# Kernel tuning notes

Hardware: AMD Instinct MI355X
Metric: run time of the kernel (lower is better)

The kernel has to match this reference:

```python
import jax, jax.numpy as jnp
import numpy as np

N_NODES = 100000
N_EDGES = 3200000
IN_DIM = 3
HID = 8
OUT_DIM = 1


def setup_inputs() -> dict:
    key = jax.random.key(0)
    ks = jax.random.split(key, 10)
    x = jax.random.normal(ks[0], (N_NODES, IN_DIM), dtype=jnp.float32)
    edge_index = jax.random.randint(ks[1], (2, N_EDGES), 0, N_NODES, dtype=jnp.int64)
    cat_dim = 2 * (HID + IN_DIM)  # 22
    s = lambda fan_in: 1.0 / np.sqrt(fan_in)
    W_in = jax.random.uniform(ks[2], (IN_DIM, HID), jnp.float32, -s(IN_DIM), s(IN_DIM))
    b_in = jnp.zeros((HID,), jnp.float32)
    W1 = jax.random.uniform(ks[3], (cat_dim, HID), jnp.float32, -s(cat_dim), s(cat_dim))
    b1 = jnp.zeros((HID,), jnp.float32)
    W2 = jax.random.uniform(ks[4], (HID, HID), jnp.float32, -s(HID), s(HID))
    b2 = jnp.zeros((HID,), jnp.float32)
    W_e = jax.random.uniform(ks[5], (cat_dim, OUT_DIM), jnp.float32, -s(cat_dim), s(cat_dim))
    b_e = jnp.zeros((OUT_DIM,), jnp.float32)
    return {"x": x, "edge_index": edge_index, "W_in": W_in, "b_in": b_in,
            "W1": W1, "b1": b1, "W2": W2, "b2": b2, "W_e": W_e, "b_e": b_e}


def reference(x, edge_index, W_in, b_in, W1, b1, W2, b2, W_e, b_e):
    src = edge_index[0]  # j (source)
    dst = edge_index[1]  # i (target)

    # inputnet: Linear + Tanh
    H = jnp.tanh(x @ W_in + b_in)               # [N, HID]
    feat = jnp.concatenate([H, x], axis=-1)      # [N, HID+IN_DIM]

    # One EdgeConv iteration (n_iters=1): message = nn(cat([x_i, x_j - x_i]))
    xi = feat[dst]                                # [E, 11]
    xj = feat[src]                                # [E, 11]
    e = jnp.concatenate([xi, xj - xi], axis=-1)   # [E, 22]
    m = jax.nn.sigmoid(e @ W1 + b1)               # [E, HID]
    m = jax.nn.sigmoid(m @ W2 + b2)               # [E, HID]
    H = jax.ops.segment_sum(m, dst, num_segments=N_NODES)  # scatter-add to targets
    feat = jnp.concatenate([H, x], axis=-1)       # [N, 11]

    # edgenetwork on concatenated endpoint features
    ef = jnp.concatenate([feat[src], feat[dst]], axis=-1)   # [E, 22]
    out = jax.nn.sigmoid(ef @ W_e + b_e)          # [E, 1]
    return out.squeeze(-1)                        # [E]
```

## Files before the change

kernel.cpp:

```cpp
#include <hip/hip_runtime.h>
#include <hip/hip_fp16.h>

#define TPB     256
#define BSH     9
#define BW      512
#define EPB     8192
#define NBMAX   256
#define S_SPLIT 16
#define FXS     2097152.0f
#define FXSI    (1.0f / 2097152.0f)

static __device__ __forceinline__ float sigmoidf(float v) {
    return __builtin_amdgcn_rcpf(1.0f + __expf(-v));
}

static __device__ __forceinline__ void unpack8(uint4 u, float o[8]) {
    union { unsigned int u; __half2 h; } c0, c1, c2, c3;
    c0.u = u.x; c1.u = u.y; c2.u = u.z; c3.u = u.w;
    float2 f0 = __half22float2(c0.h), f1 = __half22float2(c1.h);
    float2 f2 = __half22float2(c2.h), f3 = __half22float2(c3.h);
    o[0]=f0.x; o[1]=f0.y; o[2]=f1.x; o[3]=f1.y;
    o[4]=f2.x; o[5]=f2.y; o[6]=f3.x; o[7]=f3.y;
}

__global__ void k_prep(const float* __restrict__ x,
                       const float* __restrict__ W_in,
                       const float* __restrict__ b_in,
                       const float* __restrict__ W1,
                       const float* __restrict__ b1,
                       float* __restrict__ gi,
                       __half* __restrict__ gjh,
                       const int* __restrict__ dst,
                       int* __restrict__ raw,
                       int n_nodes, int n_edges, int NB, int NBLK) {
    __shared__ int cnt[NBMAX];
    int t = threadIdx.x;
    if ((int)blockIdx.x < NBLK) {
        for (int b = t; b < NB; b += TPB) cnt[b] = 0;
        __syncthreads();
        int e0 = blockIdx.x * EPB;
#pragma unroll
        for (int k = 0; k < EPB / (TPB * 4); ++k) {
            int e = e0 + k * TPB * 4 + t * 4;
            if (e + 3 < n_edges) {
                int4 d4 = *(const int4*)(dst + e);
                atomicAdd(&cnt[d4.x >> BSH], 1);
                atomicAdd(&cnt[d4.y >> BSH], 1);
                atomicAdd(&cnt[d4.z >> BSH], 1);
                atomicAdd(&cnt[d4.w >> BSH], 1);
            } else {
                int qe = min(e + 4, n_edges);
                for (int q = e; q < qe; ++q)
                    atomicAdd(&cnt[dst[q] >> BSH], 1);
            }
        }
        __syncthreads();
        for (int b = t; b < NB; b += TPB)
            raw[(size_t)blockIdx.x * NB + b] = cnt[b];
    } else {
        int n = ((int)blockIdx.x - NBLK) * TPB + t;
        if (n >= n_nodes) return;
        float x0 = x[3*n], x1 = x[3*n+1], x2 = x[3*n+2];
        float f[11];
#pragma unroll
        for (int c = 0; c < 8; ++c)
            f[c] = tanhf(b_in[c] + x0*W_in[c] + x1*W_in[8+c] + x2*W_in[16+c]);
        f[8] = x0; f[9] = x1; f[10] = x2;
        float giv[8], gjv[8];
#pragma unroll
        for (int h = 0; h < 8; ++h) {
            float vi = b1[h], vj = 0.0f;
#pragma unroll
            for (int k = 0; k < 11; ++k) {
                float wa = W1[k*8+h], wb = W1[(11+k)*8+h];
                vi += f[k] * (wa - wb);
                vj += f[k] * wb;
            }
            giv[h] = vi; gjv[h] = vj;
        }
        float4* gip = (float4*)(gi + (size_t)n * 8);
        gip[0] = make_float4(giv[0], giv[1], giv[2], giv[3]);
        gip[1] = make_float4(giv[4], giv[5], giv[6], giv[7]);
        __align__(16) __half hj[8];
#pragma unroll
        for (int k = 0; k < 8; ++k) hj[k] = __float2half_rn(gjv[k]);
        *(uint4*)(gjh + (size_t)n * 8) = *(const uint4*)hj;
    }
}

__global__ void k_scan_cols(const int* __restrict__ raw, int* __restrict__ rel,
                            int* __restrict__ totals, int NB, int NBLK) {
    __shared__ int s[TPB];
    int b = blockIdx.x, t = threadIdx.x;
    int carry = 0;
    for (int q = 0; q < NBLK; q += TPB) {
        int blk = q + t;
        int v = (blk < NBLK) ? raw[(size_t)blk * NB + b] : 0;
        __syncthreads();
        s[t] = v; __syncthreads();
        for (int o = 1; o < TPB; o <<= 1) {
            int u = (t >= o) ? s[t - o] : 0;
            __syncthreads();
            s[t] += u;
            __syncthreads();
        }
        if (blk < NBLK) rel[(size_t)blk * NB + b] = carry + s[t] - v;
        carry += s[TPB - 1];
    }
    if (t == 0) totals[b] = carry;
}

static __device__ __forceinline__ void base_scan(const int* __restrict__ totals,
                                                 int* s, int* sbase, int NB, int t) {
    int v = (t < NB) ? ((totals[t] + 3) & ~3) : 0;
    s[t] = v; __syncthreads();
    for (int o = 1; o < TPB; o <<= 1) {
        int u = (t >= o) ? s[t - o] : 0;
        __syncthreads();
        s[t] += u;
        __syncthreads();
    }
    if (t < NB) sbase[t] = s[t] - v;
    __syncthreads();
}

__launch_bounds__(TPB)
__global__ void k_scatter(const int* __restrict__ src, const int* __restrict__ dst,
                          const int* __restrict__ raw, const int* __restrict__ rel,
                          const int* __restrict__ totals,
                          int* __restrict__ sorted, int n_edges, int NB) {
    __shared__ int stage[EPB];
    __shared__ int cnt[NBMAX];
    __shared__ int lscan[NBMAX];
    __shared__ int gd[NBMAX];
    __shared__ int sbase[NBMAX];
    __shared__ int s[TPB];
    int t = threadIdx.x;

    base_scan(totals, s, sbase, NB, t);

    {
        int v = (t < NB) ? raw[(size_t)blockIdx.x * NB + t] : 0;
        __syncthreads();
        s[t] = v; __syncthreads();
        for (int o = 1; o < TPB; o <<= 1) {
            int u = (t >= o) ? s[t - o] : 0;
            __syncthreads();
            s[t] += u;
            __syncthreads();
        }
        if (t < NB) {
            lscan[t] = s[t] - v;
            cnt[t]   = s[t] - v;
            gd[t]    = sbase[t] + rel[(size_t)blockIdx.x * NB + t];
        }
    }
    __syncthreads();

    int e0 = blockIdx.x * EPB;
#pragma unroll
    for (int k = 0; k < EPB / (TPB * 4); ++k) {
        int e = e0 + k * TPB * 4 + t * 4;
        if (e + 3 < n_edges) {
            int4 s4 = *(const int4*)(src + e);
            int4 d4 = *(const int4*)(dst + e);
            int p;
            p = atomicAdd(&cnt[d4.x >> BSH], 1); stage[p] = (s4.x << BSH) | (d4.x & (BW-1));
            p = atomicAdd(&cnt[d4.y >> BSH], 1); stage[p] = (s4.y << BSH) | (d4.y & (BW-1));
            p = atomicAdd(&cnt[d4.z >> BSH], 1); stage[p] = (s4.z << BSH) | (d4.z & (BW-1));
            p = atomicAdd(&cnt[d4.w >> BSH], 1); stage[p] = (s4.w << BSH) | (d4.w & (BW-1));
        } else {
            int qe = min(e + 4, n_edges);
            for (int q = e; q < qe; ++q) {
                int d = dst[q];
                int p = atomicAdd(&cnt[d >> BSH], 1);
                stage[p] = (src[q] << BSH) | (d & (BW - 1));
            }
        }
    }
    __syncthreads();

    int wid = t >> 6, lane = t & 63;
    for (int b = wid; b < NB; b += (TPB / 64)) {
        int ls = lscan[b];
        int le = cnt[b];
        int g0 = gd[b];
        for (int i = ls + lane; i < le; i += 64)
            sorted[g0 + (i - ls)] = stage[i];
    }
}

__launch_bounds__(TPB, 4)
__global__ void k_bucket(const int* __restrict__ sorted,
                         const int* __restrict__ totals,
                         const float* __restrict__ gi, const __half* __restrict__ gjh,
                         const float* __restrict__ W2, const float* __restrict__ b2,
                         const float* __restrict__ W_e,
                         float* __restrict__ part, int n_nodes, int NB, int NBP) {
    __shared__ int sa[BW], sc[BW];
    __shared__ int sbase[NBMAX];
    __shared__ int s[TPB];
    int t = threadIdx.x;
    int sl = blockIdx.x / NBP;
    int b  = blockIdx.x - sl * NBP;

    base_scan(totals, s, sbase, NB, t);
    if (b >= NB) return;

    int nb0 = b * BW;
    for (int i = t; i < BW; i += TPB) { sa[i] = 0; sc[i] = 0; }
    __syncthreads();

    int beg = sbase[b];
    int len = totals[b];
    int qs = (((len + S_SPLIT - 1) / S_SPLIT) + 3) & ~3;
    int s0 = beg + sl * qs;
    int s1 = min(beg + len, s0 + qs);

    for (int g = s0 + t * 4; g < s1; g += TPB * 4) {
        if (g + 4 <= s1) {
            int4 pp = *(const int4*)(sorted + g);
            int d[4]  = { pp.x & (BW-1), pp.y & (BW-1), pp.z & (BW-1), pp.w & (BW-1) };
            int sj[4] = { pp.x >> BSH,   pp.y >> BSH,   pp.z >> BSH,   pp.w >> BSH };
            float ej[4][8];
#pragma unroll
            for (int q = 0; q < 4; ++q)
                unpack8(*(const uint4*)(gjh + (size_t)sj[q] * 8), ej[q]);
            float m[4][8];
#pragma unroll
            for (int q = 0; q < 4; ++q) {
                const float4* ip = (const float4*)(gi + (size_t)(nb0 + d[q]) * 8);
                float4 A = ip[0], B = ip[1];
                float ei[8] = {A.x,A.y,A.z,A.w,B.x,B.y,B.z,B.w};
#pragma unroll
                for (int k = 0; k < 8; ++k)
                    m[q][k] = sigmoidf(ei[k] + ej[q][k]);
            }
            float pa[4] = {0,0,0,0}, pc[4] = {0,0,0,0};
#pragma unroll
            for (int h = 0; h < 8; ++h) {
                float bb = b2[h];
                float v[4] = {bb, bb, bb, bb};
#pragma unroll
                for (int k = 0; k < 8; ++k) {
                    float w = W2[k*8+h];
#pragma unroll
                    for (int q = 0; q < 4; ++q) v[q] += m[q][k] * w;
                }
                float wa = W_e[h], wc = W_e[11+h];
#pragma unroll
                for (int q = 0; q < 4; ++q) {
                    float z = sigmoidf(v[q]);
                    pa[q] += z * wa; pc[q] += z * wc;
                }
            }
#pragma unroll
            for (int q = 0; q < 4; ++q) {
                atomicAdd(&sa[d[q]], __float2int_rn(pa[q] * FXS));
                atomicAdd(&sc[d[q]], __float2int_rn(pc[q] * FXS));
            }
        } else {
            for (int e = g; e < s1; ++e) {
                int p = sorted[e];
                int dl = p & (BW - 1);
                float ej[8];
                unpack8(*(const uint4*)(gjh + (size_t)(p >> BSH) * 8), ej);
                const float4* ip = (const float4*)(gi + (size_t)(nb0 + dl) * 8);
                float4 A = ip[0], B = ip[1];
                float ei[8] = {A.x,A.y,A.z,A.w,B.x,B.y,B.z,B.w};
                float m[8];
#pragma unroll
                for (int k = 0; k < 8; ++k) m[k] = sigmoidf(ei[k] + ej[k]);
                float pa = 0, pc = 0;
#pragma unroll
                for (int h = 0; h < 8; ++h) {
                    float v = b2[h];
#pragma unroll
                    for (int k = 0; k < 8; ++k) v += m[k] * W2[k*8+h];
                    float z = sigmoidf(v);
                    pa += z * W_e[h]; pc += z * W_e[11+h];
                }
                atomicAdd(&sa[dl], __float2int_rn(pa * FXS));
                atomicAdd(&sc[dl], __float2int_rn(pc * FXS));
            }
        }
    }
    __syncthreads();
    size_t row = (size_t)blockIdx.x * (2 * BW);
    for (int i = t; i < BW; i += TPB) {
        part[row + i]      = (float)sa[i] * FXSI;
        part[row + BW + i] = (float)sc[i] * FXSI;
    }
}

__global__ void k_acc(const float* __restrict__ part, const float* __restrict__ x,
                      const float* __restrict__ W_e, float* __restrict__ ac,
                      int n_nodes, int NBP) {
    int n = blockIdx.x * blockDim.x + threadIdx.x;
    if (n >= n_nodes) return;
    int b = n >> BSH, r = n & (BW - 1);
    float a = 0.0f, c = 0.0f;
#pragma unroll
    for (int s = 0; s < S_SPLIT; ++s) {
        const float* pp = part + ((size_t)(s * NBP + b)) * (2 * BW);
        a += pp[r];
        c += pp[BW + r];
    }
    float x0 = x[3*n], x1 = x[3*n+1], x2 = x[3*n+2];
    a += x0 * W_e[8]  + x1 * W_e[9]  + x2 * W_e[10];
    c += x0 * W_e[19] + x1 * W_e[20] + x2 * W_e[21];
    ac[2*n]     = a;
    ac[2*n + 1] = c;
}

__global__ void k_out2(const int* __restrict__ src, const int* __restrict__ dst,
                       const float* __restrict__ ac, const float* __restrict__ b_e,
                       float* __restrict__ out, int n_edges) {
    float bb = b_e[0];
    int e = (blockIdx.x * blockDim.x + threadIdx.x) * 4;
    if (e + 3 < n_edges) {
        int4 s4 = *(const int4*)(src + e);
        int4 d4 = *(const int4*)(dst + e);
        float4 o;
        o.x = sigmoidf(ac[2*s4.x] + ac[2*d4.x + 1] + bb);
        o.y = sigmoidf(ac[2*s4.y] + ac[2*d4.y + 1] + bb);
        o.z = sigmoidf(ac[2*s4.z] + ac[2*d4.z + 1] + bb);
        o.w = sigmoidf(ac[2*s4.w] + ac[2*d4.w + 1] + bb);
        *(float4*)(out + e) = o;
    } else {
        for (int q = e; q < n_edges; ++q)
            out[q] = sigmoidf(ac[2*src[q]] + ac[2*dst[q] + 1] + bb);
    }
}

__global__ void k_nodes(const float* __restrict__ x, const float* __restrict__ W_in,
                        const float* __restrict__ b_in, float* __restrict__ feat,
                        float* __restrict__ H2, int n_nodes) {
    int i = blockIdx.x * blockDim.x + threadIdx.x;
    if (i >= n_nodes) return;
    float x0 = x[3*i], x1 = x[3*i+1], x2 = x[3*i+2];
    float h[8];
#pragma unroll
    for (int c = 0; c < 8; ++c)
        h[c] = tanhf(b_in[c] + x0*W_in[c] + x1*W_in[8+c] + x2*W_in[16+c]);
    float4* fp = (float4*)(feat + (size_t)i * 12);
    fp[0] = make_float4(h[0],h[1],h[2],h[3]);
    fp[1] = make_float4(h[4],h[5],h[6],h[7]);
    fp[2] = make_float4(x0,x1,x2,0.0f);
    float4* hp = (float4*)(H2 + (size_t)i * 8);
    hp[0] = make_float4(0,0,0,0); hp[1] = make_float4(0,0,0,0);
}

__global__ void k_edges(const int* __restrict__ src, const int* __restrict__ dst,
                        const float* __restrict__ feat, const float* __restrict__ W1,
                        const float* __restrict__ b1, const float* __restrict__ W2,
                        const float* __restrict__ b2, float* __restrict__ H2,
                        int n_edges) {
    __shared__ float sW1[176], sW2[64], sb1[8], sb2[8];
    for (int t = threadIdx.x; t < 176; t += blockDim.x) sW1[t] = W1[t];
    for (int t = threadIdx.x; t < 64;  t += blockDim.x) sW2[t] = W2[t];
    if (threadIdx.x < 8) { sb1[threadIdx.x]=b1[threadIdx.x]; sb2[threadIdx.x]=b2[threadIdx.x]; }
    __syncthreads();
    int e = blockIdx.x * blockDim.x + threadIdx.x;
    if (e >= n_edges) return;
    int j = src[e], i = dst[e];
    const float4* fi = (const float4*)(feat + (size_t)i * 12);
    const float4* fj = (const float4*)(feat + (size_t)j * 12);
    float4 i0=fi[0],i1=fi[1],i2=fi[2],j0=fj[0],j1=fj[1],j2=fj[2];
    float xi[11]={i0.x,i0.y,i0.z,i0.w,i1.x,i1.y,i1.z,i1.w,i2.x,i2.y,i2.z};
    float xj[11]={j0.x,j0.y,j0.z,j0.w,j1.x,j1.y,j1.z,j1.w,j2.x,j2.y,j2.z};
    float dd[11];
#pragma unroll
    for (int k = 0; k < 11; ++k) dd[k]=xj[k]-xi[k];
    float m[8];
#pragma unroll
    for (int h = 0; h < 8; ++h) {
        float v = sb1[h];
#pragma unroll
        for (int k = 0; k < 11; ++k) v += xi[k]*sW1[k*8+h];
#pragma unroll
        for (int k = 0; k < 11; ++k) v += dd[k]*sW1[(11+k)*8+h];
        m[h] = sigmoidf(v);
    }
    float m2[8];
#pragma unroll
    for (int h = 0; h < 8; ++h) {
        float v = sb2[h];
#pragma unroll
        for (int k = 0; k < 8; ++k) v += m[k]*sW2[k*8+h];
        m2[h] = sigmoidf(v);
    }
    float* hp = H2 + (size_t)i * 8;
#pragma unroll
    for (int h = 0; h < 8; ++h) atomicAdd(hp + h, m2[h]);
}

__global__ void k_out(const int* __restrict__ src, const int* __restrict__ dst,
                      const float* __restrict__ H2, const float* __restrict__ x,
                      const float* __restrict__ W_e, const float* __restrict__ b_e,
                      float* __restrict__ out, int n_edges) {
    __shared__ float sW[22]; __shared__ float sb;
    if (threadIdx.x < 22) sW[threadIdx.x] = W_e[threadIdx.x];
    if (threadIdx.x == 0) sb = b_e[0];
    __syncthreads();
    int e = blockIdx.x * blockDim.x + threadIdx.x;
    if (e >= n_edges) return;
    int j = src[e], i = dst[e];
    const float4* hj = (const float4*)(H2 + (size_t)j * 8);
    const float4* hi = (const float4*)(H2 + (size_t)i * 8);
    float4 a0=hj[0],a1=hj[1],c0=hi[0],c1=hi[1];
    float acc = sb;
    acc += a0.x*sW[0]+a0.y*sW[1]+a0.z*sW[2]+a0.w*sW[3];
    acc += a1.x*sW[4]+a1.y*sW[5]+a1.z*sW[6]+a1.w*sW[7];
    acc += x[3*(size_t)j]*sW[8]+x[3*(size_t)j+1]*sW[9]+x[3*(size_t)j+2]*sW[10];
    acc += c0.x*sW[11]+c0.y*sW[12]+c0.z*sW[13]+c0.w*sW[14];
    acc += c1.x*sW[15]+c1.y*sW[16]+c1.z*sW[17]+c1.w*sW[18];
    acc += x[3*(size_t)i]*sW[19]+x[3*(size_t)i+1]*sW[20]+x[3*(size_t)i+2]*sW[21];
    out[e] = sigmoidf(acc);
}

extern "C" void kernel_launch(void* const* d_in, const int* in_sizes, int n_in,
                              void* d_out, int out_size, void* d_ws, size_t ws_size,
                              hipStream_t stream) {
    const float* x    = (const float*)d_in[0];
    const int*   ei   = (const int*)d_in[1];
    const float* W_in = (const float*)d_in[2];
    const float* b_in = (const float*)d_in[3];
    const float* W1   = (const float*)d_in[4];
    const float* b1   = (const float*)d_in[5];
    const float* W2   = (const float*)d_in[6];
    const float* b2   = (const float*)d_in[7];
    const float* W_e  = (const float*)d_in[8];
    const float* b_e  = (const float*)d_in[9];

    const int n_nodes = in_sizes[0] / 3;
    const int n_edges = in_sizes[1] / 2;
    const int* src = ei;
    const int* dst = ei + n_edges;
    float* out = (float*)d_out;

    const int NB   = (n_nodes + BW - 1) >> BSH;
    const int NBP  = (NB + 7) & ~7;
    const int NBLK = (n_edges + EPB - 1) / EPB;
    const int NFB  = (n_nodes + TPB - 1) / TPB;

    size_t off = 0;
    auto carve = [&](size_t bytes) { size_t o = off; off += (bytes + 255) & ~(size_t)255; return o; };
    char* ws = (char*)d_ws;
    size_t o_gi     = carve((size_t)n_nodes * 8 * 4);
    size_t o_gjh    = carve((size_t)n_nodes * 8 * 2);
    size_t o_ac     = carve((size_t)n_nodes * 2 * 4);
    size_t o_raw    = carve((size_t)NBLK * NB * 4);
    size_t o_rel    = carve((size_t)NBLK * NB * 4);
    size_t o_totals = carve((size_t)NB * 4);
    size_t o_sorted = carve(((size_t)n_edges + 4 * NBMAX) * 4);
    size_t o_part   = carve((size_t)NBP * S_SPLIT * 2 * BW * 4);
    bool fast = (off <= ws_size) && (NB <= NBMAX);

    if (fast) {
        float*  gi     = (float*)(ws + o_gi);
        __half* gjh    = (__half*)(ws + o_gjh);
        float*  ac     = (float*)(ws + o_ac);
        int*    raw    = (int*)(ws + o_raw);
        int*    rel    = (int*)(ws + o_rel);
        int*    totals = (int*)(ws + o_totals);
        int*    sorted = (int*)(ws + o_sorted);
        float*  part   = (float*)(ws + o_part);

        k_prep     <<<NBLK + NFB, TPB, 0, stream>>>(x, W_in, b_in, W1, b1, gi, gjh,
                                                    dst, raw, n_nodes, n_edges, NB, NBLK);
        k_scan_cols<<<NB, TPB, 0, stream>>>(raw, rel, totals, NB, NBLK);
        k_scatter  <<<NBLK, TPB, 0, stream>>>(src, dst, raw, rel, totals, sorted, n_edges, NB);
        k_bucket   <<<NBP * S_SPLIT, TPB, 0, stream>>>(sorted, totals, gi, gjh, W2, b2, W_e,
                                                       part, n_nodes, NB, NBP);
        k_acc      <<<(n_nodes + TPB - 1) / TPB, TPB, 0, stream>>>(part, x, W_e, ac, n_nodes, NBP);
        k_out2     <<<(n_edges / 4 + TPB - 1) / TPB + 1, TPB, 0, stream>>>(src, dst, ac, b_e, out, n_edges);
    } else {
        float* feat = (float*)d_ws;
        float* H2   = feat + (size_t)n_nodes * 12;
        k_nodes<<<(n_nodes + TPB - 1) / TPB, TPB, 0, stream>>>(x, W_in, b_in, feat, H2, n_nodes);
        k_edges<<<(n_edges + TPB - 1) / TPB, TPB, 0, stream>>>(src, dst, feat, W1, b1, W2, b2, H2, n_edges);
        k_out  <<<(n_edges + TPB - 1) / TPB, TPB, 0, stream>>>(src, dst, H2, x, W_e, b_e, out, n_edges);
    }
}
```

Before: 103.8 us.

## Precompute node exponentials for edge sigmoid and hoist bucket-base scan into own kernel

Node prep now stores exp(-v) for the dst and src first-layer pre-activations, so each edge's first sigmoid becomes a multiply plus reciprocal instead of an exp per element. The repeated per-block prefix scan of bucket totals is moved into a single tiny kernel whose result all blocks read. Partial sums stay as fixed-point ints and are converted to float once in the accumulate step. Storing exp(-vj) in fp16 risks overflow or precision loss for large pre-activations, and an extra kernel launch is added.

Result: faster. 100.00 us (-3.6%).

```diff
diff --git a/kernel.cpp b/kernel.cpp
--- a/kernel.cpp
+++ b/kernel.cpp
@@ -28,8 +28,8 @@
                        const float* __restrict__ b_in,
                        const float* __restrict__ W1,
                        const float* __restrict__ b1,
-                       float* __restrict__ gi,
-                       __half* __restrict__ gjh,
+                       float* __restrict__ egi,
+                       __half* __restrict__ egjh,
                        const int* __restrict__ dst,
                        int* __restrict__ raw,
                        int n_nodes, int n_edges, int NB, int NBLK) {
@@ -76,15 +76,15 @@
                 vi += f[k] * (wa - wb);
                 vj += f[k] * wb;
             }
-            giv[h] = vi; gjv[h] = vj;
-        }
-        float4* gip = (float4*)(gi + (size_t)n * 8);
+            giv[h] = __expf(-vi); gjv[h] = __expf(-vj);
+        }
+        float4* gip = (float4*)(egi + (size_t)n * 8);
         gip[0] = make_float4(giv[0], giv[1], giv[2], giv[3]);
         gip[1] = make_float4(giv[4], giv[5], giv[6], giv[7]);
         __align__(16) __half hj[8];
 #pragma unroll
         for (int k = 0; k < 8; ++k) hj[k] = __float2half_rn(gjv[k]);
-        *(uint4*)(gjh + (size_t)n * 8) = *(const uint4*)hj;
+        *(uint4*)(egjh + (size_t)n * 8) = *(const uint4*)hj;
     }
 }
 
@@ -110,38 +110,35 @@
     if (t == 0) totals[b] = carry;
 }
 
-static __device__ __forceinline__ void base_scan(const int* __restrict__ totals,
-                                                 int* s, int* sbase, int NB, int t) {
+__global__ void k_base(const int* __restrict__ totals, int* __restrict__ base,
+                       int NB) {
+    __shared__ int s[NBMAX];
+    int t = threadIdx.x;
     int v = (t < NB) ? ((totals[t] + 3) & ~3) : 0;
     s[t] = v; __syncthreads();
-    for (int o = 1; o < TPB; o <<= 1) {
+    for (int o = 1; o < NBMAX; o <<= 1) {
         int u = (t >= o) ? s[t - o] : 0;
         __syncthreads();
         s[t] += u;
         __syncthreads();
     }
-    if (t < NB) sbase[t] = s[t] - v;
-    __syncthreads();
+    if (t < NB) base[t] = s[t] - v;
 }
 
 __launch_bounds__(TPB)
 __global__ void k_scatter(const int* __restrict__ src, const int* __restrict__ dst,
                           const int* __restrict__ raw, const int* __restrict__ rel,
-                          const int* __restrict__ totals,
+                          const int* __restrict__ base,
                           int* __restrict__ sorted, int n_edges, int NB) {
     __shared__ int stage[EPB];
     __shared__ int cnt[NBMAX];
     __shared__ int lscan[NBMAX];
     __shared__ int gd[NBMAX];
-    __shared__ int sbase[NBMAX];
     __shared__ int s[TPB];
     int t = threadIdx.x;
 
-    base_scan(totals, s, sbase, NB, t);
-
     {
         int v = (t < NB) ? raw[(size_t)blockIdx.x * NB + t] : 0;
-        __syncthreads();
         s[t] = v; __syncthreads();
         for (int o = 1; o < TPB; o <<= 1) {
             int u = (t >= o) ? s[t - o] : 0;
@@ -152,7 +149,7 @@
         if (t < NB) {
             lscan[t] = s[t] - v;
             cnt[t]   = s[t] - v;
-            gd[t]    = sbase[t] + rel[(size_t)blockIdx.x * NB + t];
+            gd[t]    = base[t] + rel[(size_t)blockIdx.x * NB + t];
         }
     }
     __syncthreads();
@@ -191,27 +188,23 @@
 }
 
 __launch_bounds__(TPB, 4)
-__global__ void k_bucket(const int* __restrict__ sorted,
+__global__ void k_bucket(const int* __restrict__ sorted, const int* __restrict__ base,
                          const int* __restrict__ totals,
-                         const float* __restrict__ gi, const __half* __restrict__ gjh,
+                         const float* __restrict__ egi, const __half* __restrict__ egjh,
                          const float* __restrict__ W2, const float* __restrict__ b2,
                          const float* __restrict__ W_e,
-                         float* __restrict__ part, int n_nodes, int NB, int NBP) {
+                         int* __restrict__ part, int n_nodes, int NB, int NBP) {
     __shared__ int sa[BW], sc[BW];
-    __shared__ int sbase[NBMAX];
-    __shared__ int s[TPB];
     int t = threadIdx.x;
     int sl = blockIdx.x / NBP;
     int b  = blockIdx.x - sl * NBP;
-
-    base_scan(totals, s, sbase, NB, t);
     if (b >= NB) return;
 
     int nb0 = b * BW;
     for (int i = t; i < BW; i += TPB) { sa[i] = 0; sc[i] = 0; }
     __syncthreads();
 
-    int beg = sbase[b];
+    int beg = base[b];
     int len = totals[b];
     int qs = (((len + S_SPLIT - 1) / S_SPLIT) + 3) & ~3;
     int s0 = beg + sl * qs;
@@ -225,16 +218,16 @@
             float ej[4][8];
 #pragma unroll
             for (int q = 0; q < 4; ++q)
-                unpack8(*(const uint4*)(gjh + (size_t)sj[q] * 8), ej[q]);
+                unpack8(*(const uint4*)(egjh + (size_t)sj[q] * 8), ej[q]);
             float m[4][8];
 #pragma unroll
             for (int q = 0; q < 4; ++q) {
-                const float4* ip = (const float4*)(gi + (size_t)(nb0 + d[q]) * 8);
+                const float4* ip = (const float4*)(egi + (size_t)(nb0 + d[q]) * 8);
                 float4 A = ip[0], B = ip[1];
                 float ei[8] = {A.x,A.y,A.z,A.w,B.x,B.y,B.z,B.w};
 #pragma unroll
                 for (int k = 0; k < 8; ++k)
-                    m[q][k] = sigmoidf(ei[k] + ej[q][k]);
+                    m[q][k] = __builtin_amdgcn_rcpf(1.0f + ei[k] * ej[q][k]);
             }
             float pa[4] = {0,0,0,0}, pc[4] = {0,0,0,0};
 #pragma unroll
@@ -264,13 +257,14 @@
                 int p = sorted[e];
                 int dl = p & (BW - 1);
                 float ej[8];
-                unpack8(*(const uint4*)(gjh + (size_t)(p >> BSH) * 8), ej);
-                const float4* ip = (const float4*)(gi + (size_t)(nb0 + dl) * 8);
+                unpack8(*(const uint4*)(egjh + (size_t)(p >> BSH) * 8), ej);
+                const float4* ip = (const float4*)(egi + (size_t)(nb0 + dl) * 8);
                 float4 A = ip[0], B = ip[1];
                 float ei[8] = {A.x,A.y,A.z,A.w,B.x,B.y,B.z,B.w};
                 float m[8];
 #pragma unroll
-                for (int k = 0; k < 8; ++k) m[k] = sigmoidf(ei[k] + ej[k]);
+                for (int k = 0; k < 8; ++k)
+                    m[k] = __builtin_amdgcn_rcpf(1.0f + ei[k] * ej[k]);
                 float pa = 0, pc = 0;
 #pragma unroll
                 for (int h = 0; h < 8; ++h) {
@@ -288,24 +282,25 @@
     __syncthreads();
     size_t row = (size_t)blockIdx.x * (2 * BW);
     for (int i = t; i < BW; i += TPB) {
-        part[row + i]      = (float)sa[i] * FXSI;
-        part[row + BW + i] = (float)sc[i] * FXSI;
-    }
-}
-
-__global__ void k_acc(const float* __restrict__ part, const float* __restrict__ x,
+        part[row + i]      = sa[i];
+        part[row + BW + i] = sc[i];
+    }
+}
+
+__global__ void k_acc(const int* __restrict__ part, const float* __restrict__ x,
                       const float* __restrict__ W_e, float* __restrict__ ac,
                       int n_nodes, int NBP) {
     int n = blockIdx.x * blockDim.x + threadIdx.x;
     if (n >= n_nodes) return;
     int b = n >> BSH, r = n & (BW - 1);
-    float a = 0.0f, c = 0.0f;
+    int ia = 0, ic = 0;
 #pragma unroll
     for (int s = 0; s < S_SPLIT; ++s) {
-        const float* pp = part + ((size_t)(s * NBP + b)) * (2 * BW);
-        a += pp[r];
-        c += pp[BW + r];
-    }
+        const int* pp = part + ((size_t)(s * NBP + b)) * (2 * BW);
+        ia += pp[r];
+        ic += pp[BW + r];
+    }
+    float a = (float)ia * FXSI, c = (float)ic * FXSI;
     float x0 = x[3*n], x1 = x[3*n+1], x2 = x[3*n+2];
     a += x0 * W_e[8]  + x1 * W_e[9]  + x2 * W_e[10];
     c += x0 * W_e[19] + x1 * W_e[20] + x2 * W_e[21];
@@ -447,31 +442,34 @@
     size_t off = 0;
     auto carve = [&](size_t bytes) { size_t o = off; off += (bytes + 255) & ~(size_t)255; return o; };
     char* ws = (char*)d_ws;
-    size_t o_gi     = carve((size_t)n_nodes * 8 * 4);
-    size_t o_gjh    = carve((size_t)n_nodes * 8 * 2);
+    size_t o_egi    = carve((size_t)n_nodes * 8 * 4);
+    size_t o_egjh   = carve((size_t)n_nodes * 8 * 2);
     size_t o_ac     = carve((size_t)n_nodes * 2 * 4);
     size_t o_raw    = carve((size_t)NBLK * NB * 4);
     size_t o_rel    = carve((size_t)NBLK * NB * 4);
     size_t o_totals = carve((size_t)NB * 4);
+    size_t o_base   = carve(((size_t)NB + 1) * 4);
     size_t o_sorted = carve(((size_t)n_edges + 4 * NBMAX) * 4);
     size_t o_part   = carve((size_t)NBP * S_SPLIT * 2 * BW * 4);
     bool fast = (off <= ws_size) && (NB <= NBMAX);
 
     if (fast) {
-        float*  gi     = (float*)(ws + o_gi);
-        __half* gjh    = (__half*)(ws + o_gjh);
+        float*  egi    = (float*)(ws + o_egi);
+        __half* egjh   = (__half*)(ws + o_egjh);
         float*  ac     = (float*)(ws + o_ac);
         int*    raw    = (int*)(ws + o_raw);
         int*    rel    = (int*)(ws + o_rel);
         int*    totals = (int*)(ws + o_totals);
+        int*    base   = (int*)(ws + o_base);
         int*    sorted = (int*)(ws + o_sorted);
-        float*  part   = (float*)(ws + o_part);
-
-        k_prep     <<<NBLK + NFB, TPB, 0, stream>>>(x, W_in, b_in, W1, b1, gi, gjh,
+        int*    part   = (int*)(ws + o_part);
+
+        k_prep     <<<NBLK + NFB, TPB, 0, stream>>>(x, W_in, b_in, W1, b1, egi, egjh,
                                                     dst, raw, n_nodes, n_edges, NB, NBLK);
         k_scan_cols<<<NB, TPB, 0, stream>>>(raw, rel, totals, NB, NBLK);
-        k_scatter  <<<NBLK, TPB, 0, stream>>>(src, dst, raw, rel, totals, sorted, n_edges, NB);
-        k_bucket   <<<NBP * S_SPLIT, TPB, 0, stream>>>(sorted, totals, gi, gjh, W2, b2, W_e,
+        k_base     <<<1, NBMAX, 0, stream>>>(totals, base, NB);
+        k_scatter  <<<NBLK, TPB, 0, stream>>>(src, dst, raw, rel, base, sorted, n_edges, NB);
+        k_bucket   <<<NBP * S_SPLIT, TPB, 0, stream>>>(sorted, base, totals, egi, egjh, W2, b2, W_e,
                                                        part, n_nodes, NB, NBP);
         k_acc      <<<(n_nodes + TPB - 1) / TPB, TPB, 0, stream>>>(part, x, W_e, ac, n_nodes, NBP);
         k_out2     <<<(n_edges / 4 + TPB - 1) / TPB + 1, TPB, 0, stream>>>(src, dst, ac, b_e, out, n_edges);
```
